# Optimization experiments

Hardware: AMD Instinct MI355X
Metric: run time of the kernel (lower is better)

Reference implementation:

```python
import jax, jax.numpy as jnp
import numpy as np

# pywt 'db4' analysis filters (dec_lo, dec_hi)
DEC_LO = np.array([-0.010597401784997278, 0.032883011666982945, 0.030841381835986965,
                   -0.18703481171888114, -0.02798376941698385, 0.6308807679295904,
                   0.7148465705525415, 0.23037781330885523], dtype=np.float32)
DEC_HI = np.array([-0.23037781330885523, 0.7148465705525415, -0.6308807679295904,
                   -0.02798376941698385, 0.18703481171888114, 0.030841381835986965,
                   -0.032883011666982945, -0.010597401784997278], dtype=np.float32)
J = 3          # dwt levels for subwindow_size=64 with db4
DWT_LEN = 84   # 14 (lo) + 35 + 21 + 14 (his)
NEG_SLOPE = 1e-3
FILT = np.stack([DEC_LO[::-1].copy(), DEC_HI[::-1].copy()])[:, None, :]  # [2,1,8] reversed, as in pytorch_wavelets


def _afb1d(x):
    # Single-level analysis filter bank along last axis, reflect padding (pytorch_wavelets mode='reflect')
    N = x.shape[-1]
    L = 8
    outsize = (N + L - 1) // 2
    p = 2 * (outsize - 1) - N + L
    xp = jnp.pad(x, [(0, 0)] * (x.ndim - 1) + [(p // 2, (p + 1) // 2)], mode='reflect')
    lead = x.shape[:-1]
    xr = xp.reshape((-1, 1, xp.shape[-1]))
    out = jax.lax.conv_general_dilated(xr, jnp.asarray(FILT, dtype=x.dtype), (2,), 'VALID')  # [B,2,outsize]
    lo = out[:, 0].reshape(lead + (outsize,))
    hi = out[:, 1].reshape(lead + (outsize,))
    return lo, hi


def _dwt(x):
    # J-level DWT; returns concat([lo_J, hi_1, ..., hi_J], axis=-1), matching [x_lo]+x_hi cat order
    his = []
    lo = x
    for _ in range(J):
        lo, hi = _afb1d(lo)
        his.append(hi)
    return jnp.concatenate([lo] + his, axis=-1)


def setup_inputs() -> dict:
    key = jax.random.key(0)
    k1, k2, k3 = jax.random.split(key, 3)
    B, K = 16384, 16
    x = jax.random.normal(k1, (B, 1, 64, 8, 8), dtype=jnp.float32)
    conv_w = jax.random.normal(k2, (K, 1, DWT_LEN, 8, 8), dtype=jnp.float32) * (1.0 / np.sqrt(DWT_LEN * 64))
    conv_b = jax.random.normal(k3, (K,), dtype=jnp.float32) * 0.01
    return {"x": x, "conv_w": conv_w, "conv_b": conv_b}


def reference(x, conv_w, conv_b):
    # x: [B,1,T=64,8,8]; time_interval=1, no maxpool, subwindow_nbins=1 (subwindow = full window)
    xt = jnp.moveaxis(x, 2, -1)            # [B,1,8,8,T] -> DWT along time
    d = _dwt(xt)                           # [B,1,8,8,DWT_LEN]
    d = jnp.moveaxis(d, -1, 2)             # [B,1,DWT_LEN,8,8]
    # Conv3d with kernel spanning full [DWT_LEN,8,8] == full contraction -> [B,K]
    feat = jnp.einsum('bcdhw,kcdhw->bk', d, conv_w) + conv_b
    # Dropout3d is identity in eval; LeakyReLU(0.001) then flatten (already [B, nbins*K], nbins=1)
    return jnp.where(feat >= 0, feat, NEG_SLOPE * feat)
```

## Files before the change

kernel.cpp:

```cpp
#include <hip/hip_runtime.h>
#include <hip/hip_bf16.h>

#define DWT_LEN_C 84
#define TDIM 64
#define INNER 4096
#define KOUT 16
#define KSPLIT 8
#define QCOLS 512
#define STEPS 16

typedef __attribute__((ext_vector_type(8))) short short8;
typedef __attribute__((ext_vector_type(4))) float floatx4;

__device__ __forceinline__ unsigned short bf16_rne(float f) {
    unsigned u = __float_as_uint(f);
    unsigned r = u + 0x7fffu + ((u >> 16) & 1u);
    return (unsigned short)(r >> 16);
}

__device__ const float c_dec_lo[8] = {-0.010597401784997278f, 0.032883011666982945f, 0.030841381835986965f,
                                      -0.18703481171888114f, -0.02798376941698385f, 0.6308807679295904f,
                                      0.7148465705525415f, 0.23037781330885523f};
__device__ const float c_dec_hi[8] = {-0.23037781330885523f, 0.7148465705525415f, -0.6308807679295904f,
                                      -0.02798376941698385f, 0.18703481171888114f, 0.030841381835986965f,
                                      -0.032883011666982945f, -0.010597401784997278f};

__device__ void afb1d_col(const float* v, int N, float* lo, float* hi, int M) {
    for (int i = 0; i < M; ++i) {
        float slo = 0.f, shi = 0.f;
        for (int j = 0; j < 8; ++j) {
            int idx = 2 * i + j - 6;
            if (idx < 0) idx = -idx;
            if (idx >= N) idx = 2 * N - 2 - idx;
            float c = v[idx];
            slo = fmaf(c, c_dec_lo[7 - j], slo);
            shi = fmaf(c, c_dec_hi[7 - j], shi);
        }
        lo[i] = slo; hi[i] = shi;
    }
}

__global__ __launch_bounds__(256) void build_weff_bf16(const float* __restrict__ conv_w,
                                                       unsigned short* __restrict__ Wb) {
    __shared__ float Wd[DWT_LEN_C][TDIM];
    const int t0 = threadIdx.x;
    if (t0 < TDIM) {
        float v[64];
        for (int n = 0; n < 64; ++n) v[n] = (n == t0) ? 1.f : 0.f;
        float lo1[35], hi1[35], lo2[21], hi2[21], lo3[14], hi3[14];
        afb1d_col(v, 64, lo1, hi1, 35);
        afb1d_col(lo1, 35, lo2, hi2, 21);
        afb1d_col(lo2, 21, lo3, hi3, 14);
        for (int i = 0; i < 14; ++i) Wd[i][t0] = lo3[i];
        for (int i = 0; i < 35; ++i) Wd[14 + i][t0] = hi1[i];
        for (int i = 0; i < 21; ++i) Wd[49 + i][t0] = hi2[i];
        for (int i = 0; i < 14; ++i) Wd[70 + i][t0] = hi3[i];
    }
    __syncthreads();

    const int idx = blockIdx.x * 256 + threadIdx.x;
    const int k = idx >> 12;
    const int col = idx & 4095;
    const int t = col >> 6;
    const int hw = col & 63;
    float s = 0.f;
    const float* cw = conv_w + (size_t)k * DWT_LEN_C * 64 + hw;
#pragma unroll 4
    for (int dd = 0; dd < DWT_LEN_C; ++dd)
        s = fmaf(cw[dd * 64], Wd[dd][t], s);
    Wb[idx] = bf16_rne(s);
}

__global__ __launch_bounds__(256, 6) void dwt_mfma(const float* __restrict__ x,
                                                   const unsigned short* __restrict__ Wb,
                                                   float* __restrict__ partial, int B) {
    __shared__ __align__(16) unsigned short Wlds[KOUT * QCOLS];
    const int t = threadIdx.x;
    const int rowgroup = blockIdx.x >> 3;
    const int kq = blockIdx.x & 7;

    {
        const int n = t & 15;
        const int c0 = (t >> 4) * 32;
        const unsigned short* src = Wb + n * INNER + kq * QCOLS + c0;
#pragma unroll
        for (int g = 0; g < 4; ++g) {
            const int c = c0 + g * 8;
            *(short8*)&Wlds[n * QCOLS + (c ^ ((n & 7) * 8))] = *(const short8*)(src + g * 8);
        }
    }
    __syncthreads();

    const int lane = t & 63;
    const int wid = t >> 6;
    const int qg = lane >> 4;
    const int mrow = lane & 15;
    const int rowbase = rowgroup * 64 + wid * 16;
    const float* xrow = x + (size_t)(rowbase + mrow) * INNER + kq * QCOLS;
    const unsigned short* wrow = &Wlds[mrow * QCOLS];
    const int swz = (mrow & 7) * 8;

    floatx4 acc = {0.f, 0.f, 0.f, 0.f};
#pragma unroll 4
    for (int step = 0; step < STEPS; ++step) {
        const int col = step * 32 + qg * 8;
        const float4 lo = *(const float4*)(xrow + col);
        const float4 hi = *(const float4*)(xrow + col + 4);
        short8 a;
        a[0] = (short)bf16_rne(lo.x); a[1] = (short)bf16_rne(lo.y);
        a[2] = (short)bf16_rne(lo.z); a[3] = (short)bf16_rne(lo.w);
        a[4] = (short)bf16_rne(hi.x); a[5] = (short)bf16_rne(hi.y);
        a[6] = (short)bf16_rne(hi.z); a[7] = (short)bf16_rne(hi.w);
        const short8 b = *(const short8*)(wrow + (col ^ swz));
        acc = __builtin_amdgcn_mfma_f32_16x16x32_bf16(a, b, acc, 0, 0, 0);
    }

    const int orow = rowbase + qg * 4;
    float* pq = partial + (size_t)kq * B * KOUT;
#pragma unroll
    for (int r = 0; r < 4; ++r)
        pq[(size_t)(orow + r) * KOUT + mrow] = acc[r];
}

__global__ __launch_bounds__(256) void finish(const float* __restrict__ partial,
                                              const float* __restrict__ bias,
                                              float* __restrict__ out, int B) {
    const int idx4 = (blockIdx.x * 256 + threadIdx.x) * 4;
    if (idx4 >= B * KOUT) return;
    const size_t stride = (size_t)B * KOUT;
    float4 s = *(const float4*)(partial + idx4);
#pragma unroll
    for (int kq = 1; kq < KSPLIT; ++kq) {
        float4 p = *(const float4*)(partial + kq * stride + idx4);
        s.x += p.x; s.y += p.y; s.z += p.z; s.w += p.w;
    }
    const float4 bb = *(const float4*)(bias + (idx4 & 15));
    s.x += bb.x; s.y += bb.y; s.z += bb.z; s.w += bb.w;
    s.x = (s.x >= 0.f) ? s.x : 1e-3f * s.x;
    s.y = (s.y >= 0.f) ? s.y : 1e-3f * s.y;
    s.z = (s.z >= 0.f) ? s.z : 1e-3f * s.z;
    s.w = (s.w >= 0.f) ? s.w : 1e-3f * s.w;
    *(float4*)(out + idx4) = s;
}

extern "C" void kernel_launch(void* const* d_in, const int* in_sizes, int n_in,
                              void* d_out, int out_size, void* d_ws, size_t ws_size,
                              hipStream_t stream) {
    const float* x      = (const float*)d_in[0];
    const float* conv_w = (const float*)d_in[1];
    const float* conv_b = (const float*)d_in[2];
    float* out = (float*)d_out;
    const int B = in_sizes[0] / INNER;

    float* partial = (float*)d_ws;
    unsigned short* Wb = (unsigned short*)((char*)d_ws + ((size_t)16 << 20));

    build_weff_bf16<<<(KOUT * INNER) / 256, 256, 0, stream>>>(conv_w, Wb);
    dwt_mfma<<<(B / 64) * KSPLIT, 256, 0, stream>>>(x, Wb, partial, B);
    finish<<<(B * KOUT / 4 + 255) / 256, 256, 0, stream>>>(partial, conv_b, out, B);
}
```

Baseline: 59.11 us.

## Reduce K-split to two halves and double-buffer x loads in registers

Each block now covers half of the 4096-wide inner dimension instead of an eighth, so the weight tile staged in LDS grows to 64KB and there are 4x fewer partial sums for the finish kernel to reduce. The main loop is restructured into ping-pong register buffers, each holding eight float4 loads, so global loads for the next chunk are issued before the MFMAs on the current chunk. The larger LDS footprint and extra registers lower occupancy and leave fewer blocks in flight, which may reduce latency hiding on this bandwidth-bound read of x.

```diff
diff --git a/kernel.cpp b/kernel.cpp
--- a/kernel.cpp
+++ b/kernel.cpp
@@ -5,9 +5,9 @@
 #define TDIM 64
 #define INNER 4096
 #define KOUT 16
-#define KSPLIT 8
-#define QCOLS 512
-#define STEPS 16
+#define KSPLIT 2
+#define HCOLS 2048
+#define OITER 16
 
 typedef __attribute__((ext_vector_type(8))) short short8;
 typedef __attribute__((ext_vector_type(4))) float floatx4;
@@ -71,22 +71,22 @@
     Wb[idx] = bf16_rne(s);
 }
 
-__global__ __launch_bounds__(256, 6) void dwt_mfma(const float* __restrict__ x,
-                                                   const unsigned short* __restrict__ Wb,
-                                                   float* __restrict__ partial, int B) {
-    __shared__ __align__(16) unsigned short Wlds[KOUT * QCOLS];
+__global__ __launch_bounds__(256) void dwt_mfma(const float* __restrict__ x,
+                                                const unsigned short* __restrict__ Wb,
+                                                float* __restrict__ partial, int B) {
+    __shared__ __align__(16) unsigned short Wlds[KOUT * HCOLS];
     const int t = threadIdx.x;
-    const int rowgroup = blockIdx.x >> 3;
-    const int kq = blockIdx.x & 7;
+    const int rowgroup = blockIdx.x >> 1;
+    const int kh = blockIdx.x & 1;
 
     {
         const int n = t & 15;
-        const int c0 = (t >> 4) * 32;
-        const unsigned short* src = Wb + n * INNER + kq * QCOLS + c0;
+        const int c0 = (t >> 4) * 128;
+        const unsigned short* src = Wb + n * INNER + kh * HCOLS + c0;
 #pragma unroll
-        for (int g = 0; g < 4; ++g) {
+        for (int g = 0; g < 16; ++g) {
             const int c = c0 + g * 8;
-            *(short8*)&Wlds[n * QCOLS + (c ^ ((n & 7) * 8))] = *(const short8*)(src + g * 8);
+            *(short8*)&Wlds[n * HCOLS + (c ^ ((n & 7) * 8))] = *(const short8*)(src + g * 8);
         }
     }
     __syncthreads();
@@ -96,27 +96,53 @@
     const int qg = lane >> 4;
     const int mrow = lane & 15;
     const int rowbase = rowgroup * 64 + wid * 16;
-    const float* xrow = x + (size_t)(rowbase + mrow) * INNER + kq * QCOLS;
-    const unsigned short* wrow = &Wlds[mrow * QCOLS];
+    const float* xrow = x + (size_t)(rowbase + mrow) * INNER + kh * HCOLS + qg * 8;
+    const unsigned short* wrow = &Wlds[mrow * HCOLS];
     const int swz = (mrow & 7) * 8;
 
     floatx4 acc = {0.f, 0.f, 0.f, 0.f};
-#pragma unroll 4
-    for (int step = 0; step < STEPS; ++step) {
-        const int col = step * 32 + qg * 8;
-        const float4 lo = *(const float4*)(xrow + col);
-        const float4 hi = *(const float4*)(xrow + col + 4);
-        short8 a;
-        a[0] = (short)bf16_rne(lo.x); a[1] = (short)bf16_rne(lo.y);
-        a[2] = (short)bf16_rne(lo.z); a[3] = (short)bf16_rne(lo.w);
-        a[4] = (short)bf16_rne(hi.x); a[5] = (short)bf16_rne(hi.y);
-        a[6] = (short)bf16_rne(hi.z); a[7] = (short)bf16_rne(hi.w);
-        const short8 b = *(const short8*)(wrow + (col ^ swz));
-        acc = __builtin_amdgcn_mfma_f32_16x16x32_bf16(a, b, acc, 0, 0, 0);
+    float4 bufA[8], bufB[8];
+
+#define XLOAD(buf, it)                                                          \
+    {                                                                           \
+        const float* p = xrow + (it) * 128;                                     \
+        _Pragma("unroll")                                                       \
+        for (int s = 0; s < 4; ++s) {                                           \
+            buf[2 * s]     = *(const float4*)(p + s * 32);                      \
+            buf[2 * s + 1] = *(const float4*)(p + s * 32 + 4);                  \
+        }                                                                       \
     }
 
+#define XCOMPUTE(buf, it)                                                       \
+    {                                                                           \
+        _Pragma("unroll")                                                       \
+        for (int s = 0; s < 4; ++s) {                                           \
+            const float4 lo = buf[2 * s];                                       \
+            const float4 hi = buf[2 * s + 1];                                   \
+            short8 a;                                                           \
+            a[0] = (short)bf16_rne(lo.x); a[1] = (short)bf16_rne(lo.y);         \
+            a[2] = (short)bf16_rne(lo.z); a[3] = (short)bf16_rne(lo.w);         \
+            a[4] = (short)bf16_rne(hi.x); a[5] = (short)bf16_rne(hi.y);         \
+            a[6] = (short)bf16_rne(hi.z); a[7] = (short)bf16_rne(hi.w);         \
+            const int col = (it) * 128 + s * 32 + qg * 8;                       \
+            const short8 b = *(const short8*)(wrow + (col ^ swz));              \
+            acc = __builtin_amdgcn_mfma_f32_16x16x32_bf16(a, b, acc, 0, 0, 0);  \
+        }                                                                       \
+    }
+
+    XLOAD(bufA, 0);
+#pragma unroll 1
+    for (int it = 0; it < OITER; it += 2) {
+        XLOAD(bufB, it + 1);
+        XCOMPUTE(bufA, it);
+        if (it + 2 < OITER) XLOAD(bufA, it + 2);
+        XCOMPUTE(bufB, it + 1);
+    }
+#undef XLOAD
+#undef XCOMPUTE
+
     const int orow = rowbase + qg * 4;
-    float* pq = partial + (size_t)kq * B * KOUT;
+    float* pq = partial + (size_t)kh * B * KOUT;
 #pragma unroll
     for (int r = 0; r < 4; ++r)
         pq[(size_t)(orow + r) * KOUT + mrow] = acc[r];
@@ -130,8 +156,8 @@
     const size_t stride = (size_t)B * KOUT;
     float4 s = *(const float4*)(partial + idx4);
 #pragma unroll
-    for (int kq = 1; kq < KSPLIT; ++kq) {
-        float4 p = *(const float4*)(partial + kq * stride + idx4);
+    for (int q = 1; q < KSPLIT; ++q) {
+        float4 p = *(const float4*)(partial + q * stride + idx4);
         s.x += p.x; s.y += p.y; s.z += p.z; s.w += p.w;
     }
     const float4 bb = *(const float4*)(bias + (idx4 & 15));
@@ -153,7 +179,7 @@
     const int B = in_sizes[0] / INNER;
 
     float* partial = (float*)d_ws;
-    unsigned short* Wb = (unsigned short*)((char*)d_ws + ((size_t)16 << 20));
+    unsigned short* Wb = (unsigned short*)((char*)d_ws + ((size_t)4 << 20));
 
     build_weff_bf16<<<(KOUT * INNER) / 256, 256, 0, stream>>>(conv_w, Wb);
     dwt_mfma<<<(B / 64) * KSPLIT, 256, 0, stream>>>(x, Wb, partial, B);
```

New measurement: 57.49 us, median of 2. -2.7%, faster.
